# Kernel optimization log

Hardware: AMD Instinct MI355X
Metric: run time of the kernel (lower is better)

The kernel has to match this reference:

```python
import jax, jax.numpy as jnp
import numpy as np

B, T, C = 4, 2048, 1024
T_PAST = 2048


def setup_inputs() -> dict:
    key = jax.random.key(0)
    ks = jax.random.split(key, 9)
    s = 1.0 / np.sqrt(C)
    return {
        "x": jax.random.normal(ks[0], (B, T, C), dtype=jnp.float32),
        "past_k": jax.random.normal(ks[1], (B, T_PAST, C), dtype=jnp.float32),
        "past_v": jax.random.normal(ks[2], (B, T_PAST, C), dtype=jnp.float32),
        "Wq": jax.random.normal(ks[3], (C, C), dtype=jnp.float32) * s,
        "bq": jnp.zeros((C,), dtype=jnp.float32),
        "Wk": jax.random.normal(ks[4], (C, C), dtype=jnp.float32) * s,
        "bk": jnp.zeros((C,), dtype=jnp.float32),
        "Wv": jax.random.normal(ks[5], (C, C), dtype=jnp.float32) * s,
        "bv": jnp.zeros((C,), dtype=jnp.float32),
    }


def reference(x, past_k, past_v, Wq, bq, Wk, bk, Wv, bv):
    Bb, Tt, Cc = x.shape
    # nn.Linear: y = x @ W^T + b
    Q = jnp.einsum('btc,dc->btd', x, Wq) + bq
    K = jnp.einsum('btc,dc->btd', x, Wk) + bk
    V = jnp.einsum('btc,dc->btd', x, Wv) + bv
    K = jnp.concatenate([past_k, K], axis=1)
    V = jnp.concatenate([past_v, V], axis=1)
    T_total = K.shape[1]
    scores = jnp.einsum('btc,bsc->bts', Q, K) / jnp.sqrt(jnp.float32(Cc))
    # Faithful to torch.tril(ones(T, T_total)): allow j <= i (even across cache)
    mask = jnp.arange(T_total)[None, :] <= jnp.arange(Tt)[:, None]
    scores = jnp.where(mask[None, :, :], scores, -jnp.inf)
    weights = jax.nn.softmax(scores, axis=-1)
    out = jnp.einsum('bts,bsc->btc', weights, V)
    return (out, K, V)
```

## Files before the change

### kernel.cpp

```cpp
#include <hip/hip_runtime.h>


typedef __bf16 bf16x8 __attribute__((ext_vector_type(8)));
typedef float f32x4 __attribute__((ext_vector_type(4)));

#define BB   4
#define TQ   2048
#define CD   1024
#define TPAST 2048
#define TTOT 4096
#define MROWS (BB * TQ)
#define SSTRIDE ((size_t)TTOT * CD * 2)

__device__ __forceinline__ unsigned short f32_to_bf16u(float f) {
  unsigned int u = __float_as_uint(f);
  u += 0x7FFFu + ((u >> 16) & 1u);
  return (unsigned short)(u >> 16);
}
__device__ __forceinline__ float bf16u_to_f32(unsigned short h) {
  unsigned int u = ((unsigned int)h) << 16;
  return __uint_as_float(u);
}
__device__ __forceinline__ unsigned int pack_bf16(float a, float b) {
  return (unsigned int)f32_to_bf16u(a) | ((unsigned int)f32_to_bf16u(b) << 16);
}

__device__ __forceinline__ void gload_lds16(const unsigned short* g,
                                            unsigned short* l) {
  __builtin_amdgcn_global_load_lds(
      (const __attribute__((address_space(1))) void*)g,
      (__attribute__((address_space(3))) void*)l, 16, 0, 0);
}

#define TP_PAD 134
#define VCT_BLOCKS 2048
#define R0_END 2097152
#define R1_END 2359296
#define R2_END 2621440
#define R3_END 2883584
#define R4_END 4980736
__global__ __launch_bounds__(256) void prep(
    const float* __restrict__ x, const float* __restrict__ wq,
    const float* __restrict__ wk, const float* __restrict__ wv,
    const float* __restrict__ pk, const float* __restrict__ pV,
    unsigned short* __restrict__ xb, unsigned short* __restrict__ wqb,
    unsigned short* __restrict__ wkb, unsigned short* __restrict__ wvb,
    unsigned short* __restrict__ kb,
    float* __restrict__ outV, unsigned short* __restrict__ VT) {
  const int tid = threadIdx.x;
  if (blockIdx.x < VCT_BLOCKS) {
    __shared__ unsigned short T[32 * TP_PAD];
    const int bid = blockIdx.x;
    const int s0 = (bid & 63) * 32, c0 = ((bid >> 6) & 7) * 128, b = bid >> 9;
    const int s = tid >> 3, i8 = tid & 7;
    const float* src = &pV[(size_t)(b * TPAST + s0 + s) * CD + c0];
    float* dst = &outV[(size_t)b * (TTOT * CD) + (size_t)(s0 + s) * CD + c0];
#pragma unroll
    for (int k = 0; k < 4; ++k) {
      int c = k * 32 + i8 * 4;
      float4 f = *(const float4*)&src[c];
      *(float4*)&dst[c] = f;
      *(unsigned int*)&T[s * TP_PAD + c]     = pack_bf16(f.x, f.y);
      *(unsigned int*)&T[s * TP_PAD + c + 2] = pack_bf16(f.z, f.w);
    }
    __syncthreads();
    const int c = tid >> 2, sq = tid & 3;
#pragma unroll
    for (int ii = 0; ii < 2; ++ii) {
      int cc = c + ii * 64;
      unsigned short tmp[8];
#pragma unroll
      for (int j = 0; j < 8; ++j) tmp[j] = T[(sq * 8 + j) * TP_PAD + cc];
      *(uint4*)&VT[(size_t)(b * CD + c0 + cc) * TPAST + s0 + sq * 8] = *(uint4*)tmp;
    }
    return;
  }
  int i = (blockIdx.x - VCT_BLOCKS) * 256 + tid;
  const float* src; unsigned short* dst; int off;
  if (i < R0_END)      { src = x;  dst = xb;  off = i; }
  else if (i < R1_END) { src = wq; dst = wqb; off = i - R0_END; }
  else if (i < R2_END) { src = wk; dst = wkb; off = i - R1_END; }
  else if (i < R3_END) { src = wv; dst = wvb; off = i - R2_END; }
  else                 { src = pk; dst = kb;  off = i - R3_END; }
  float4 f = ((const float4*)src)[off];
  uint2 o;
  o.x = pack_bf16(f.x, f.y);
  o.y = pack_bf16(f.z, f.w);
  ((uint2*)dst)[off] = o;
}

__global__ __launch_bounds__(256) void copy_past_kernel(
    const float* __restrict__ src, float* __restrict__ dst) {
  int i = blockIdx.x * 256 + threadIdx.x;
  int b = i >> 19;
  int rem = i & 524287;
  ((float4*)dst)[(size_t)b * 1048576 + rem] = ((const float4*)src)[i];
}

__global__ __launch_bounds__(256) void proj_qkv(
    const unsigned short* __restrict__ A,
    const unsigned short* __restrict__ Wq_,
    const unsigned short* __restrict__ Wv_,
    const unsigned short* __restrict__ Wk_,
    const float* __restrict__ bq_, const float* __restrict__ bv_,
    const float* __restrict__ bk_,
    unsigned short* __restrict__ outQ,
    float* __restrict__ outV,
    float* __restrict__ outK) {
  __shared__ unsigned short sA[2][128 * 32];
  __shared__ unsigned short sB[2][128 * 32];
  const int tm = blockIdx.x * 128;
  const int which = blockIdx.y >> 3;
  const int tn = (blockIdx.y & 7) * 128;
  const unsigned short* W = (which == 0) ? Wq_ : (which == 1) ? Wv_ : Wk_;
  const float* bias = (which == 0) ? bq_ : (which == 1) ? bv_ : bk_;
  const int tid = threadIdx.x, lane = tid & 63, wv = tid >> 6;
  const int wr = wv >> 1, wc = wv & 1;
  const int gr = lane >> 2, gc = (lane & 3) * 8;
  const unsigned short* aSrc = &A[(size_t)(tm + wv * 32 + gr) * CD + gc];
  const unsigned short* bSrc = &W[(size_t)(tn + wv * 32 + gr) * CD + gc];
  const int ldsOff = wv * 32 * 32;
  f32x4 acc[4][4] = {};
  const int NT = CD / 32;
  gload_lds16(aSrc, &sA[0][ldsOff]);
  gload_lds16(aSrc + (size_t)16 * CD, &sA[0][ldsOff + 16 * 32]);
  gload_lds16(bSrc, &sB[0][ldsOff]);
  gload_lds16(bSrc + (size_t)16 * CD, &sB[0][ldsOff + 16 * 32]);
  __syncthreads();
  for (int t = 0; t < NT; ++t) {
    const int cur = t & 1;
    if (t + 1 < NT) {
      const int k0 = (t + 1) * 32, nb = cur ^ 1;
      gload_lds16(aSrc + k0, &sA[nb][ldsOff]);
      gload_lds16(aSrc + k0 + (size_t)16 * CD, &sA[nb][ldsOff + 16 * 32]);
      gload_lds16(bSrc + k0, &sB[nb][ldsOff]);
      gload_lds16(bSrc + k0 + (size_t)16 * CD, &sB[nb][ldsOff + 16 * 32]);
    }
    bf16x8 af[4], bg[4];
    const int koff = (lane >> 4) * 8;
#pragma unroll
    for (int i = 0; i < 4; ++i)
      af[i] = *(const bf16x8*)&sA[cur][(wr * 64 + i * 16 + (lane & 15)) * 32 + koff];
#pragma unroll
    for (int i = 0; i < 4; ++i)
      bg[i] = *(const bf16x8*)&sB[cur][(wc * 64 + i * 16 + (lane & 15)) * 32 + koff];
#pragma unroll
    for (int mi = 0; mi < 4; ++mi)
#pragma unroll
      for (int ni = 0; ni < 4; ++ni)
        acc[mi][ni] = __builtin_amdgcn_mfma_f32_16x16x32_bf16(
            af[mi], bg[ni], acc[mi][ni], 0, 0, 0);
    __syncthreads();
  }
  const int rsub = (lane >> 4) * 4, csub = lane & 15;
#pragma unroll
  for (int mi = 0; mi < 4; ++mi)
#pragma unroll
    for (int ni = 0; ni < 4; ++ni) {
      int gcn = tn + wc * 64 + ni * 16 + csub;
      float bvv = bias[gcn];
#pragma unroll
      for (int r = 0; r < 4; ++r) {
        int grw = tm + wr * 64 + mi * 16 + rsub + r;
        float v = acc[mi][ni][r] + bvv;
        if (which == 0) {
          outQ[(size_t)grw * CD + gcn] = f32_to_bf16u(v * 0.03125f);
        } else {
          int b = grw >> 11, t = grw & (TQ - 1);
          float* o = (which == 1) ? outV : outK;
          o[(size_t)b * (TTOT * CD) + (size_t)(TPAST + t) * CD + gcn] = v;
        }
      }
    }
}

__global__ __launch_bounds__(256) void score_gemm(
    const unsigned short* __restrict__ Q,
    const unsigned short* __restrict__ KB,
    unsigned short* __restrict__ S16) {
  const int t0 = blockIdx.x * 128, s0 = blockIdx.y * 128, b = blockIdx.z;
  if (s0 > t0 + 127) return;
  __shared__ unsigned short sA[2][128 * 32];
  __shared__ unsigned short sB[2][128 * 32];
  const int tid = threadIdx.x, lane = tid & 63, wv = tid >> 6;
  const int wr = wv >> 1, wc = wv & 1;
  const int gr = lane >> 2, gc = (lane & 3) * 8;
  const unsigned short* aSrc = &Q[(size_t)(b * TQ + t0 + wv * 32 + gr) * CD + gc];
  const unsigned short* bSrc = &KB[(size_t)(b * TPAST + s0 + wv * 32 + gr) * CD + gc];
  const int ldsOff = wv * 32 * 32;
  f32x4 acc[4][4] = {};
  const int NT = CD / 32;
  gload_lds16(aSrc, &sA[0][ldsOff]);
  gload_lds16(aSrc + (size_t)16 * CD, &sA[0][ldsOff + 16 * 32]);
  gload_lds16(bSrc, &sB[0][ldsOff]);
  gload_lds16(bSrc + (size_t)16 * CD, &sB[0][ldsOff + 16 * 32]);
  __syncthreads();
  for (int t = 0; t < NT; ++t) {
    const int cur = t & 1;
    if (t + 1 < NT) {
      const int k0 = (t + 1) * 32, nb = cur ^ 1;
      gload_lds16(aSrc + k0, &sA[nb][ldsOff]);
      gload_lds16(aSrc + k0 + (size_t)16 * CD, &sA[nb][ldsOff + 16 * 32]);
      gload_lds16(bSrc + k0, &sB[nb][ldsOff]);
      gload_lds16(bSrc + k0 + (size_t)16 * CD, &sB[nb][ldsOff + 16 * 32]);
    }
    bf16x8 af[4], bg[4];
    const int koff = (lane >> 4) * 8;
#pragma unroll
    for (int i = 0; i < 4; ++i)
      af[i] = *(const bf16x8*)&sA[cur][(wr * 64 + i * 16 + (lane & 15)) * 32 + koff];
#pragma unroll
    for (int i = 0; i < 4; ++i)
      bg[i] = *(const bf16x8*)&sB[cur][(wc * 64 + i * 16 + (lane & 15)) * 32 + koff];
#pragma unroll
    for (int mi = 0; mi < 4; ++mi)
#pragma unroll
      for (int ni = 0; ni < 4; ++ni)
        acc[mi][ni] = __builtin_amdgcn_mfma_f32_16x16x32_bf16(
            af[mi], bg[ni], acc[mi][ni], 0, 0, 0);
    __syncthreads();
  }
  const int rsub = (lane >> 4) * 4, csub = lane & 15;
#pragma unroll
  for (int mi = 0; mi < 4; ++mi)
#pragma unroll
    for (int ni = 0; ni < 4; ++ni) {
      int gs = s0 + wc * 64 + ni * 16 + csub;
#pragma unroll
      for (int r = 0; r < 4; ++r) {
        int gt = t0 + wr * 64 + mi * 16 + rsub + r;
        S16[(size_t)b * SSTRIDE + (size_t)gt * TPAST + gs] =
            f32_to_bf16u(acc[mi][ni][r]);
      }
    }
}

__global__ __launch_bounds__(256) void softmax_kernel(unsigned short* __restrict__ S16) {
  const int row = blockIdx.x;
  const int b = row >> 11, t = row & (TQ - 1);
  unsigned short* p = S16 + (size_t)b * SSTRIDE + (size_t)t * TPAST;
  const int tid = threadIdx.x, lane = tid & 63, wv = tid >> 6;
  __shared__ float red[8];
  const int base = tid * 8;
  uint4 raw = *(const uint4*)&p[base];
  const unsigned short* rw = (const unsigned short*)&raw;
  float v[8];
  float m = -3.0e38f;
#pragma unroll
  for (int i = 0; i < 8; ++i) {
    v[i] = (base + i <= t) ? bf16u_to_f32(rw[i]) : -3.0e38f;
    m = fmaxf(m, v[i]);
  }
#pragma unroll
  for (int off = 32; off >= 1; off >>= 1) m = fmaxf(m, __shfl_down(m, off));
  if (lane == 0) red[wv] = m;
  __syncthreads();
  if (tid == 0) red[4] = fmaxf(fmaxf(red[0], red[1]), fmaxf(red[2], red[3]));
  __syncthreads();
  const float rm = red[4];
  float e[8], s = 0.f;
#pragma unroll
  for (int i = 0; i < 8; ++i) {
    e[i] = (base + i <= t) ? __expf(v[i] - rm) : 0.f;
    s += e[i];
  }
#pragma unroll
  for (int off = 32; off >= 1; off >>= 1) s += __shfl_down(s, off);
  __syncthreads();
  if (lane == 0) red[wv] = s;
  __syncthreads();
  if (tid == 0) red[5] = red[0] + red[1] + red[2] + red[3];
  __syncthreads();
  const float inv = 1.f / red[5];
  unsigned short ob[8];
#pragma unroll
  for (int i = 0; i < 8; ++i) ob[i] = f32_to_bf16u(e[i] * inv);
  *(uint4*)&p[base] = *(uint4*)ob;
}

__global__ __launch_bounds__(256) void pv_gemm(
    const unsigned short* __restrict__ Pb,
    const unsigned short* __restrict__ VT,
    float* __restrict__ O) {
  const int t0 = blockIdx.x * 128, c0 = blockIdx.y * 128, b = blockIdx.z;
  __shared__ unsigned short sA[2][128 * 32];
  __shared__ unsigned short sB[2][128 * 32];
  const int tid = threadIdx.x, lane = tid & 63, wv = tid >> 6;
  const int wr = wv >> 1, wc = wv & 1;
  const int gr = lane >> 2, gc = (lane & 3) * 8;
  const unsigned short* aSrc =
      &Pb[(size_t)b * SSTRIDE + (size_t)(t0 + wv * 32 + gr) * TPAST + gc];
  const unsigned short* bSrc =
      &VT[(size_t)(b * CD + c0 + wv * 32 + gr) * TPAST + gc];
  const int ldsOff = wv * 32 * 32;
  f32x4 acc[4][4] = {};
  const int s_end = (t0 + 128 < TPAST) ? (t0 + 128) : TPAST;
  const int NT = s_end / 32;
  gload_lds16(aSrc, &sA[0][ldsOff]);
  gload_lds16(aSrc + (size_t)16 * TPAST, &sA[0][ldsOff + 16 * 32]);
  gload_lds16(bSrc, &sB[0][ldsOff]);
  gload_lds16(bSrc + (size_t)16 * TPAST, &sB[0][ldsOff + 16 * 32]);
  __syncthreads();
  for (int t = 0; t < NT; ++t) {
    const int cur = t & 1;
    if (t + 1 < NT) {
      const int s0 = (t + 1) * 32, nb = cur ^ 1;
      gload_lds16(aSrc + s0, &sA[nb][ldsOff]);
      gload_lds16(aSrc + s0 + (size_t)16 * TPAST, &sA[nb][ldsOff + 16 * 32]);
      gload_lds16(bSrc + s0, &sB[nb][ldsOff]);
      gload_lds16(bSrc + s0 + (size_t)16 * TPAST, &sB[nb][ldsOff + 16 * 32]);
    }
    bf16x8 af[4], bg[4];
    const int koff = (lane >> 4) * 8;
#pragma unroll
    for (int i = 0; i < 4; ++i)
      af[i] = *(const bf16x8*)&sA[cur][(wr * 64 + i * 16 + (lane & 15)) * 32 + koff];
#pragma unroll
    for (int i = 0; i < 4; ++i)
      bg[i] = *(const bf16x8*)&sB[cur][(wc * 64 + i * 16 + (lane & 15)) * 32 + koff];
#pragma unroll
    for (int mi = 0; mi < 4; ++mi)
#pragma unroll
      for (int ni = 0; ni < 4; ++ni)
        acc[mi][ni] = __builtin_amdgcn_mfma_f32_16x16x32_bf16(
            af[mi], bg[ni], acc[mi][ni], 0, 0, 0);
    __syncthreads();
  }
  const int rsub = (lane >> 4) * 4, csub = lane & 15;
#pragma unroll
  for (int mi = 0; mi < 4; ++mi)
#pragma unroll
    for (int ni = 0; ni < 4; ++ni) {
      int gcn = c0 + wc * 64 + ni * 16 + csub;
#pragma unroll
      for (int r = 0; r < 4; ++r) {
        int gt = t0 + wr * 64 + mi * 16 + rsub + r;
        O[(size_t)(b * TQ + gt) * CD + gcn] = acc[mi][ni][r];
      }
    }
}

extern "C" void kernel_launch(void* const* d_in, const int* in_sizes, int n_in,
                              void* d_out, int out_size, void* d_ws, size_t ws_size,
                              hipStream_t stream) {
  const float* x  = (const float*)d_in[0];
  const float* pk = (const float*)d_in[1];
  const float* pv = (const float*)d_in[2];
  const float* Wq = (const float*)d_in[3];
  const float* bq = (const float*)d_in[4];
  const float* Wk = (const float*)d_in[5];
  const float* bk = (const float*)d_in[6];
  const float* Wv = (const float*)d_in[7];
  const float* bv = (const float*)d_in[8];

  float* out  = (float*)d_out;
  float* outK = out + (size_t)BB * TQ * CD;
  float* outV = outK + (size_t)BB * TTOT * CD;
  unsigned short* S16 = (unsigned short*)outK;

  unsigned short* xb  = (unsigned short*)d_ws;
  unsigned short* wqb = xb + (size_t)MROWS * CD;
  unsigned short* wkb = wqb + (size_t)CD * CD;
  unsigned short* wvb = wkb + (size_t)CD * CD;
  unsigned short* qb  = wvb + (size_t)CD * CD;
  unsigned short* vtb = qb + (size_t)MROWS * CD;
  unsigned short* kb  = vtb + (size_t)BB * CD * TPAST;

  prep<<<VCT_BLOCKS + R4_END / 256, 256, 0, stream>>>(
      x, Wq, Wk, Wv, pk, pv, xb, wqb, wkb, wvb, kb, outV, vtb);
  proj_qkv<<<dim3(MROWS / 128, 24), 256, 0, stream>>>(
      xb, wqb, wvb, wkb, bq, bv, bk, qb, outV, outK);
  score_gemm<<<dim3(TQ / 128, TPAST / 128, BB), 256, 0, stream>>>(qb, kb, S16);
  softmax_kernel<<<BB * TQ, 256, 0, stream>>>(S16);
  pv_gemm<<<dim3(TQ / 128, CD / 128, BB), 256, 0, stream>>>(S16, vtb, out);
  copy_past_kernel<<<BB * TPAST * CD / 4 / 256, 256, 0, stream>>>(pk, outK);
}
```

Baseline: 238.2 us.

## Share a triple-buffered swizzled GEMM core across projection, score and PV kernels

Replaces the double-buffered LDS loop in the three GEMM kernels with a shared core. It uses three LDS stages, explicit vmcnt waits and raw s_barrier instead of __syncthreads, and XOR-swizzles the global-to-LDS source columns to cut LDS bank conflicts on fragment reads. It also raises MFMA issue priority with setprio and sets a minimum of three blocks per CU in launch bounds. The cost is more LDS per block (48KB) and fragile hand-placed waitcnt/barrier sequencing that must stay correct across stage reuse.

New measurement: 215.8 us. -9.4%, faster.

```diff
diff --git a/kernel.cpp b/kernel.cpp
--- a/kernel.cpp
+++ b/kernel.cpp
@@ -11,6 +11,7 @@
 #define TTOT 4096
 #define MROWS (BB * TQ)
 #define SSTRIDE ((size_t)TTOT * CD * 2)
+#define SLOTU 8192
 
 __device__ __forceinline__ unsigned short f32_to_bf16u(float f) {
   unsigned int u = __float_as_uint(f);
@@ -30,6 +31,72 @@
   __builtin_amdgcn_global_load_lds(
       (const __attribute__((address_space(1))) void*)g,
       (__attribute__((address_space(3))) void*)l, 16, 0, 0);
+}
+
+struct StagePtrs {
+  const unsigned short *a0, *a1, *b0, *b1;
+};
+
+__device__ __forceinline__ void stage_step(StagePtrs& p, unsigned short* lds,
+                                           int stOff, int wv) {
+  unsigned short* base = lds + stOff + wv * 512;
+  gload_lds16(p.a0, base);
+  gload_lds16(p.a1, base + 2048);
+  gload_lds16(p.b0, base + 4096);
+  gload_lds16(p.b1, base + 6144);
+  p.a0 += 32; p.a1 += 32; p.b0 += 32; p.b1 += 32;
+}
+
+__device__ __forceinline__ void gemm_core_v2(
+    StagePtrs p, unsigned short* lds, int NT,
+    int wr, int wc, int lane, int wv, f32x4 acc[4][4]) {
+  const int gph8 = (((lane >> 4) ^ (lane & 3))) * 8;
+  const int aRd = (wr * 64 + (lane & 15)) * 32 + gph8;
+  const int bRd = 4096 + (wc * 64 + (lane & 15)) * 32 + gph8;
+
+  stage_step(p, lds, 0, wv);
+  stage_step(p, lds, SLOTU, wv);
+  int stOff = 2 * SLOTU;
+  int rdOff = 0;
+
+  for (int t = 0; t < NT; ++t) {
+    if (t + 2 < NT) {
+      stage_step(p, lds, stOff, wv);
+      stOff = (stOff == 2 * SLOTU) ? 0 : stOff + SLOTU;
+    }
+    const int rem = NT - 1 - t;
+    if (rem >= 2)      asm volatile("s_waitcnt vmcnt(8)" ::: "memory");
+    else if (rem == 1) asm volatile("s_waitcnt vmcnt(4)" ::: "memory");
+    else               asm volatile("s_waitcnt vmcnt(0)" ::: "memory");
+    asm volatile("s_barrier" ::: "memory");
+    bf16x8 af[4], bg[4];
+#pragma unroll
+    for (int i = 0; i < 4; ++i)
+      af[i] = *(const bf16x8*)&lds[rdOff + aRd + i * 512];
+#pragma unroll
+    for (int i = 0; i < 4; ++i)
+      bg[i] = *(const bf16x8*)&lds[rdOff + bRd + i * 512];
+    asm volatile("s_waitcnt lgkmcnt(0)" ::: "memory");
+    __builtin_amdgcn_sched_barrier(0);
+    asm volatile("s_barrier" ::: "memory");
+    __builtin_amdgcn_s_setprio(1);
+#pragma unroll
+    for (int mi = 0; mi < 4; ++mi)
+#pragma unroll
+      for (int ni = 0; ni < 4; ++ni)
+        acc[mi][ni] = __builtin_amdgcn_mfma_f32_16x16x32_bf16(
+            af[mi], bg[ni], acc[mi][ni], 0, 0, 0);
+    __builtin_amdgcn_s_setprio(0);
+    rdOff = (rdOff == 2 * SLOTU) ? 0 : rdOff + SLOTU;
+  }
+}
+
+__device__ __forceinline__ const unsigned short* swz_src(
+    const unsigned short* base, size_t rowStart, size_t ld,
+    int part, int wv, int lane) {
+  int row = part * 64 + wv * 16 + (lane >> 2);
+  int gp = (lane & 3) ^ ((lane >> 2) & 3);
+  return base + (rowStart + row) * ld + gp * 8;
 }
 
 #define TP_PAD 134
@@ -97,7 +164,7 @@
   ((float4*)dst)[(size_t)b * 1048576 + rem] = ((const float4*)src)[i];
 }
 
-__global__ __launch_bounds__(256) void proj_qkv(
+__global__ __launch_bounds__(256, 3) void proj_qkv(
     const unsigned short* __restrict__ A,
     const unsigned short* __restrict__ Wq_,
     const unsigned short* __restrict__ Wv_,
@@ -105,10 +172,8 @@
     const float* __restrict__ bq_, const float* __restrict__ bv_,
     const float* __restrict__ bk_,
     unsigned short* __restrict__ outQ,
-    float* __restrict__ outV,
-    float* __restrict__ outK) {
-  __shared__ unsigned short sA[2][128 * 32];
-  __shared__ unsigned short sB[2][128 * 32];
+    float* __restrict__ outV, float* __restrict__ outK) {
+  __shared__ unsigned short lds[3 * SLOTU];
   const int tm = blockIdx.x * 128;
   const int which = blockIdx.y >> 3;
   const int tn = (blockIdx.y & 7) * 128;
@@ -116,42 +181,13 @@
   const float* bias = (which == 0) ? bq_ : (which == 1) ? bv_ : bk_;
   const int tid = threadIdx.x, lane = tid & 63, wv = tid >> 6;
   const int wr = wv >> 1, wc = wv & 1;
-  const int gr = lane >> 2, gc = (lane & 3) * 8;
-  const unsigned short* aSrc = &A[(size_t)(tm + wv * 32 + gr) * CD + gc];
-  const unsigned short* bSrc = &W[(size_t)(tn + wv * 32 + gr) * CD + gc];
-  const int ldsOff = wv * 32 * 32;
+  StagePtrs p;
+  p.a0 = swz_src(A, tm, CD, 0, wv, lane);
+  p.a1 = swz_src(A, tm, CD, 1, wv, lane);
+  p.b0 = swz_src(W, tn, CD, 0, wv, lane);
+  p.b1 = swz_src(W, tn, CD, 1, wv, lane);
   f32x4 acc[4][4] = {};
-  const int NT = CD / 32;
-  gload_lds16(aSrc, &sA[0][ldsOff]);
-  gload_lds16(aSrc + (size_t)16 * CD, &sA[0][ldsOff + 16 * 32]);
-  gload_lds16(bSrc, &sB[0][ldsOff]);
-  gload_lds16(bSrc + (size_t)16 * CD, &sB[0][ldsOff + 16 * 32]);
-  __syncthreads();
-  for (int t = 0; t < NT; ++t) {
-    const int cur = t & 1;
-    if (t + 1 < NT) {
-      const int k0 = (t + 1) * 32, nb = cur ^ 1;
-      gload_lds16(aSrc + k0, &sA[nb][ldsOff]);
-      gload_lds16(aSrc + k0 + (size_t)16 * CD, &sA[nb][ldsOff + 16 * 32]);
-      gload_lds16(bSrc + k0, &sB[nb][ldsOff]);
-      gload_lds16(bSrc + k0 + (size_t)16 * CD, &sB[nb][ldsOff + 16 * 32]);
-    }
-    bf16x8 af[4], bg[4];
-    const int koff = (lane >> 4) * 8;
-#pragma unroll
-    for (int i = 0; i < 4; ++i)
-      af[i] = *(const bf16x8*)&sA[cur][(wr * 64 + i * 16 + (lane & 15)) * 32 + koff];
-#pragma unroll
-    for (int i = 0; i < 4; ++i)
-      bg[i] = *(const bf16x8*)&sB[cur][(wc * 64 + i * 16 + (lane & 15)) * 32 + koff];
-#pragma unroll
-    for (int mi = 0; mi < 4; ++mi)
-#pragma unroll
-      for (int ni = 0; ni < 4; ++ni)
-        acc[mi][ni] = __builtin_amdgcn_mfma_f32_16x16x32_bf16(
-            af[mi], bg[ni], acc[mi][ni], 0, 0, 0);
-    __syncthreads();
-  }
+  gemm_core_v2(p, lds, CD / 32, wr, wc, lane, wv, acc);
   const int rsub = (lane >> 4) * 4, csub = lane & 15;
 #pragma unroll
   for (int mi = 0; mi < 4; ++mi)
@@ -174,52 +210,22 @@
     }
 }
 
-__global__ __launch_bounds__(256) void score_gemm(
+__global__ __launch_bounds__(256, 3) void score_gemm(
     const unsigned short* __restrict__ Q,
     const unsigned short* __restrict__ KB,
     unsigned short* __restrict__ S16) {
   const int t0 = blockIdx.x * 128, s0 = blockIdx.y * 128, b = blockIdx.z;
   if (s0 > t0 + 127) return;
-  __shared__ unsigned short sA[2][128 * 32];
-  __shared__ unsigned short sB[2][128 * 32];
+  __shared__ unsigned short lds[3 * SLOTU];
   const int tid = threadIdx.x, lane = tid & 63, wv = tid >> 6;
   const int wr = wv >> 1, wc = wv & 1;
-  const int gr = lane >> 2, gc = (lane & 3) * 8;
-  const unsigned short* aSrc = &Q[(size_t)(b * TQ + t0 + wv * 32 + gr) * CD + gc];
-  const unsigned short* bSrc = &KB[(size_t)(b * TPAST + s0 + wv * 32 + gr) * CD + gc];
-  const int ldsOff = wv * 32 * 32;
+  StagePtrs p;
+  p.a0 = swz_src(Q, (size_t)b * TQ + t0, CD, 0, wv, lane);
+  p.a1 = swz_src(Q, (size_t)b * TQ + t0, CD, 1, wv, lane);
+  p.b0 = swz_src(KB, (size_t)b * TPAST + s0, CD, 0, wv, lane);
+  p.b1 = swz_src(KB, (size_t)b * TPAST + s0, CD, 1, wv, lane);
   f32x4 acc[4][4] = {};
-  const int NT = CD / 32;
-  gload_lds16(aSrc, &sA[0][ldsOff]);
-  gload_lds16(aSrc + (size_t)16 * CD, &sA[0][ldsOff + 16 * 32]);
-  gload_lds16(bSrc, &sB[0][ldsOff]);
-  gload_lds16(bSrc + (size_t)16 * CD, &sB[0][ldsOff + 16 * 32]);
-  __syncthreads();
-  for (int t = 0; t < NT; ++t) {
-    const int cur = t & 1;
-    if (t + 1 < NT) {
-      const int k0 = (t + 1) * 32, nb = cur ^ 1;
-      gload_lds16(aSrc + k0, &sA[nb][ldsOff]);
-      gload_lds16(aSrc + k0 + (size_t)16 * CD, &sA[nb][ldsOff + 16 * 32]);
-      gload_lds16(bSrc + k0, &sB[nb][ldsOff]);
-      gload_lds16(bSrc + k0 + (size_t)16 * CD, &sB[nb][ldsOff + 16 * 32]);
-    }
-    bf16x8 af[4], bg[4];
-    const int koff = (lane >> 4) * 8;
-#pragma unroll
-    for (int i = 0; i < 4; ++i)
-      af[i] = *(const bf16x8*)&sA[cur][(wr * 64 + i * 16 + (lane & 15)) * 32 + koff];
-#pragma unroll
-    for (int i = 0; i < 4; ++i)
-      bg[i] = *(const bf16x8*)&sB[cur][(wc * 64 + i * 16 + (lane & 15)) * 32 + koff];
-#pragma unroll
-    for (int mi = 0; mi < 4; ++mi)
-#pragma unroll
-      for (int ni = 0; ni < 4; ++ni)
-        acc[mi][ni] = __builtin_amdgcn_mfma_f32_16x16x32_bf16(
-            af[mi], bg[ni], acc[mi][ni], 0, 0, 0);
-    __syncthreads();
-  }
+  gemm_core_v2(p, lds, CD / 32, wr, wc, lane, wv, acc);
   const int rsub = (lane >> 4) * 4, csub = lane & 15;
 #pragma unroll
   for (int mi = 0; mi < 4; ++mi)
@@ -278,54 +284,22 @@
   *(uint4*)&p[base] = *(uint4*)ob;
 }
 
-__global__ __launch_bounds__(256) void pv_gemm(
+__global__ __launch_bounds__(256, 3) void pv_gemm(
     const unsigned short* __restrict__ Pb,
     const unsigned short* __restrict__ VT,
     float* __restrict__ O) {
   const int t0 = blockIdx.x * 128, c0 = blockIdx.y * 128, b = blockIdx.z;
-  __shared__ unsigned short sA[2][128 * 32];
-  __shared__ unsigned short sB[2][128 * 32];
+  __shared__ unsigned short lds[3 * SLOTU];
   const int tid = threadIdx.x, lane = tid & 63, wv = tid >> 6;
   const int wr = wv >> 1, wc = wv & 1;
-  const int gr = lane >> 2, gc = (lane & 3) * 8;
-  const unsigned short* aSrc =
-      &Pb[(size_t)b * SSTRIDE + (size_t)(t0 + wv * 32 + gr) * TPAST + gc];
-  const unsigned short* bSrc =
-      &VT[(size_t)(b * CD + c0 + wv * 32 + gr) * TPAST + gc];
-  const int ldsOff = wv * 32 * 32;
+  StagePtrs p;
+  p.a0 = swz_src(Pb + (size_t)b * SSTRIDE, t0, TPAST, 0, wv, lane);
+  p.a1 = swz_src(Pb + (size_t)b * SSTRIDE, t0, TPAST, 1, wv, lane);
+  p.b0 = swz_src(VT, (size_t)b * CD + c0, TPAST, 0, wv, lane);
+  p.b1 = swz_src(VT, (size_t)b * CD + c0, TPAST, 1, wv, lane);
   f32x4 acc[4][4] = {};
   const int s_end = (t0 + 128 < TPAST) ? (t0 + 128) : TPAST;
-  const int NT = s_end / 32;
-  gload_lds16(aSrc, &sA[0][ldsOff]);
-  gload_lds16(aSrc + (size_t)16 * TPAST, &sA[0][ldsOff + 16 * 32]);
-  gload_lds16(bSrc, &sB[0][ldsOff]);
-  gload_lds16(bSrc + (size_t)16 * TPAST, &sB[0][ldsOff + 16 * 32]);
-  __syncthreads();
-  for (int t = 0; t < NT; ++t) {
-    const int cur = t & 1;
-    if (t + 1 < NT) {
-      const int s0 = (t + 1) * 32, nb = cur ^ 1;
-      gload_lds16(aSrc + s0, &sA[nb][ldsOff]);
-      gload_lds16(aSrc + s0 + (size_t)16 * TPAST, &sA[nb][ldsOff + 16 * 32]);
-      gload_lds16(bSrc + s0, &sB[nb][ldsOff]);
-      gload_lds16(bSrc + s0 + (size_t)16 * TPAST, &sB[nb][ldsOff + 16 * 32]);
-    }
-    bf16x8 af[4], bg[4];
-    const int koff = (lane >> 4) * 8;
-#pragma unroll
-    for (int i = 0; i < 4; ++i)
-      af[i] = *(const bf16x8*)&sA[cur][(wr * 64 + i * 16 + (lane & 15)) * 32 + koff];
-#pragma unroll
-    for (int i = 0; i < 4; ++i)
-      bg[i] = *(const bf16x8*)&sB[cur][(wc * 64 + i * 16 + (lane & 15)) * 32 + koff];
-#pragma unroll
-    for (int mi = 0; mi < 4; ++mi)
-#pragma unroll
-      for (int ni = 0; ni < 4; ++ni)
-        acc[mi][ni] = __builtin_amdgcn_mfma_f32_16x16x32_bf16(
-            af[mi], bg[ni], acc[mi][ni], 0, 0, 0);
-    __syncthreads();
-  }
+  gemm_core_v2(p, lds, s_end / 32, wr, wc, lane, wv, acc);
   const int rsub = (lane >> 4) * 4, csub = lane & 15;
 #pragma unroll
   for (int mi = 0; mi < 4; ++mi)
```
